# Optimization experiments

Hardware: AMD Instinct MI355X
Metric: run time of the kernel (lower is better)

## Reference

```python
import jax, jax.numpy as jnp
import numpy as np

N = 128           # hidden size n
SIGMA_REC = 0.15  # sigma_rec from __init__


def setup_inputs() -> dict:
    key = jax.random.key(0)
    ks = jax.random.split(key, 6)
    B, T, I, O = 128, 3000, 6, 2
    u = jax.random.normal(ks[0], (B, T, I), jnp.float32)
    p = jax.random.normal(ks[1], (B, N), jnp.float32)
    noise = jax.random.normal(ks[2], (B, T, N), jnp.float32)  # unit normal; scaled in reference
    W_rec = jax.random.normal(ks[3], (N, N), jnp.float32) / jnp.sqrt(jnp.float32(N))
    W_in = jax.random.normal(ks[4], (N, I), jnp.float32) / jnp.sqrt(jnp.float32(I))
    W_out = jax.random.normal(ks[5], (O, N), jnp.float32) / jnp.sqrt(jnp.float32(N))
    alpha = jnp.full((1,), 0.2, jnp.float32)  # dt/tau Euler step
    return dict(u=u, p=p, alpha=alpha, noise=noise, W_rec=W_rec, W_in=W_in, W_out=W_out)


def reference(u, p, alpha, noise, W_rec, W_in, W_out):
    B, T, _ = u.shape
    a = alpha.reshape(())
    scale = jnp.sqrt(2.0 * a * SIGMA_REC ** 2)
    # Precompute the non-recurrent drive for steps 0..T-2, time-major: [T-1, B, N]
    drive = (jnp.einsum('bti,ni->tbn', u[:, :-1], W_in)
             + scale * jnp.swapaxes(noise[:, :-1], 0, 1)
             + p[None, :, :])
    x0 = jnp.zeros((B, N), u.dtype)

    def step(x, d):
        x_new = (1.0 - a) * x + a * jax.nn.relu(x @ W_rec.T + d)
        return x_new, x_new

    _, xs = jax.lax.scan(step, x0, drive)              # xs: [T-1, B, N]
    states = jnp.swapaxes(jnp.concatenate([x0[None], xs], axis=0), 0, 1)  # [B, T, N]
    out = jnp.einsum('btn,on->bto', jax.nn.relu(states), W_out)           # [B, T, 2]
    return out, states
```

## Files before the change

### kernel.cpp

```cpp
#include <hip/hip_runtime.h>
#include <math.h>

#define NH 128
#define NI 6
#define SIGMA_REC 0.15f
#define NCHUNK 8
#define WARM 384

typedef __fp16 h2v __attribute__((ext_vector_type(2)));
typedef unsigned int vu4 __attribute__((ext_vector_type(4)));

__device__ __forceinline__ unsigned int pkh(float a, float b) {
    h2v h = __builtin_amdgcn_cvt_pkrtz(a, b);
    return __builtin_bit_cast(unsigned int, h);
}
#define H2(u) __builtin_bit_cast(h2v, (unsigned int)(u))

struct U6 { float2 a, b, c; };

#define LDWH(r) vu4 w##r##_0, w##r##_1, w##r##_2, w##r##_3, \
                    w##r##_4, w##r##_5, w##r##_6, w##r##_7; { \
    const float4* qp = reinterpret_cast<const float4*>( \
        W_rec + (size_t)(n0 + (r)) * NH + 64 * h); \
    float4 f0 = qp[0],  f1 = qp[1],  f2 = qp[2],  f3 = qp[3]; \
    float4 f4 = qp[4],  f5 = qp[5],  f6 = qp[6],  f7 = qp[7]; \
    float4 f8 = qp[8],  f9 = qp[9],  fA = qp[10], fB = qp[11]; \
    float4 fC = qp[12], fD = qp[13], fE = qp[14], fF = qp[15]; \
    w##r##_0 = (vu4){pkh(f0.x,f0.y), pkh(f0.z,f0.w), pkh(f1.x,f1.y), pkh(f1.z,f1.w)}; \
    w##r##_1 = (vu4){pkh(f2.x,f2.y), pkh(f2.z,f2.w), pkh(f3.x,f3.y), pkh(f3.z,f3.w)}; \
    w##r##_2 = (vu4){pkh(f4.x,f4.y), pkh(f4.z,f4.w), pkh(f5.x,f5.y), pkh(f5.z,f5.w)}; \
    w##r##_3 = (vu4){pkh(f6.x,f6.y), pkh(f6.z,f6.w), pkh(f7.x,f7.y), pkh(f7.z,f7.w)}; \
    w##r##_4 = (vu4){pkh(f8.x,f8.y), pkh(f8.z,f8.w), pkh(f9.x,f9.y), pkh(f9.z,f9.w)}; \
    w##r##_5 = (vu4){pkh(fA.x,fA.y), pkh(fA.z,fA.w), pkh(fB.x,fB.y), pkh(fB.z,fB.w)}; \
    w##r##_6 = (vu4){pkh(fC.x,fC.y), pkh(fC.z,fC.w), pkh(fD.x,fD.y), pkh(fD.z,fD.w)}; \
    w##r##_7 = (vu4){pkh(fE.x,fE.y), pkh(fE.z,fE.w), pkh(fF.x,fF.y), pkh(fF.z,fF.w)}; }

#define ROWDOT(r) h2v acc##r; { \
    h2v t0 = __builtin_elementwise_fma(H2(w##r##_0.x), H2(xh0.x), z2); \
    h2v t1 = __builtin_elementwise_fma(H2(w##r##_0.y), H2(xh0.y), z2); \
    t0 = __builtin_elementwise_fma(H2(w##r##_0.z), H2(xh0.z), t0); \
    t1 = __builtin_elementwise_fma(H2(w##r##_0.w), H2(xh0.w), t1); \
    t0 = __builtin_elementwise_fma(H2(w##r##_1.x), H2(xh1.x), t0); \
    t1 = __builtin_elementwise_fma(H2(w##r##_1.y), H2(xh1.y), t1); \
    t0 = __builtin_elementwise_fma(H2(w##r##_1.z), H2(xh1.z), t0); \
    t1 = __builtin_elementwise_fma(H2(w##r##_1.w), H2(xh1.w), t1); \
    t0 = __builtin_elementwise_fma(H2(w##r##_2.x), H2(xh2.x), t0); \
    t1 = __builtin_elementwise_fma(H2(w##r##_2.y), H2(xh2.y), t1); \
    t0 = __builtin_elementwise_fma(H2(w##r##_2.z), H2(xh2.z), t0); \
    t1 = __builtin_elementwise_fma(H2(w##r##_2.w), H2(xh2.w), t1); \
    t0 = __builtin_elementwise_fma(H2(w##r##_3.x), H2(xh3.x), t0); \
    t1 = __builtin_elementwise_fma(H2(w##r##_3.y), H2(xh3.y), t1); \
    t0 = __builtin_elementwise_fma(H2(w##r##_3.z), H2(xh3.z), t0); \
    t1 = __builtin_elementwise_fma(H2(w##r##_3.w), H2(xh3.w), t1); \
    t0 = __builtin_elementwise_fma(H2(w##r##_4.x), H2(xh4.x), t0); \
    t1 = __builtin_elementwise_fma(H2(w##r##_4.y), H2(xh4.y), t1); \
    t0 = __builtin_elementwise_fma(H2(w##r##_4.z), H2(xh4.z), t0); \
    t1 = __builtin_elementwise_fma(H2(w##r##_4.w), H2(xh4.w), t1); \
    t0 = __builtin_elementwise_fma(H2(w##r##_5.x), H2(xh5.x), t0); \
    t1 = __builtin_elementwise_fma(H2(w##r##_5.y), H2(xh5.y), t1); \
    t0 = __builtin_elementwise_fma(H2(w##r##_5.z), H2(xh5.z), t0); \
    t1 = __builtin_elementwise_fma(H2(w##r##_5.w), H2(xh5.w), t1); \
    t0 = __builtin_elementwise_fma(H2(w##r##_6.x), H2(xh6.x), t0); \
    t1 = __builtin_elementwise_fma(H2(w##r##_6.y), H2(xh6.y), t1); \
    t0 = __builtin_elementwise_fma(H2(w##r##_6.z), H2(xh6.z), t0); \
    t1 = __builtin_elementwise_fma(H2(w##r##_6.w), H2(xh6.w), t1); \
    t0 = __builtin_elementwise_fma(H2(w##r##_7.x), H2(xh7.x), t0); \
    t1 = __builtin_elementwise_fma(H2(w##r##_7.y), H2(xh7.y), t1); \
    t0 = __builtin_elementwise_fma(H2(w##r##_7.z), H2(xh7.z), t0); \
    t1 = __builtin_elementwise_fma(H2(w##r##_7.w), H2(xh7.w), t1); \
    acc##r = t0 + t1; }

#define DOT_OCT(j, xv) \
    c00 = __builtin_amdgcn_fdot2(H2(a##j.x), H2((xv).x), c00, false); \
    c01 = __builtin_amdgcn_fdot2(H2(a##j.y), H2((xv).y), c01, false); \
    c02 = __builtin_amdgcn_fdot2(H2(a##j.z), H2((xv).z), c02, false); \
    c03 = __builtin_amdgcn_fdot2(H2(a##j.w), H2((xv).w), c03, false); \
    c10 = __builtin_amdgcn_fdot2(H2(b##j.x), H2((xv).x), c10, false); \
    c11 = __builtin_amdgcn_fdot2(H2(b##j.y), H2((xv).y), c11, false); \
    c12 = __builtin_amdgcn_fdot2(H2(b##j.z), H2((xv).z), c12, false); \
    c13 = __builtin_amdgcn_fdot2(H2(b##j.w), H2((xv).w), c13, false)

#define LDW(j) vu4 a##j, b##j; { \
    const float4* q0 = reinterpret_cast<const float4*>(wr0 + 8 * (j)); \
    const float4* q1 = reinterpret_cast<const float4*>(wr1 + 8 * (j)); \
    float4 f0 = q0[0], f1 = q0[1], g0 = q1[0], g1 = q1[1]; \
    a##j = (vu4){pkh(f0.x, f0.y), pkh(f0.z, f0.w), pkh(f1.x, f1.y), pkh(f1.z, f1.w)}; \
    b##j = (vu4){pkh(g0.x, g0.y), pkh(g0.z, g0.w), pkh(g1.x, g1.y), pkh(g1.z, g1.w)}; }

#define PIN_AB() \
    asm volatile("" : "+v"(a0), "+v"(a1), "+v"(a2),  "+v"(a3), \
                      "+v"(a4), "+v"(a5), "+v"(a6),  "+v"(a7), \
                      "+v"(a8), "+v"(a9), "+v"(a10), "+v"(a11), \
                      "+v"(a12), "+v"(a13), "+v"(a14), "+v"(a15)); \
    asm volatile("" : "+v"(b0), "+v"(b1), "+v"(b2),  "+v"(b3), \
                      "+v"(b4), "+v"(b5), "+v"(b6),  "+v"(b7), \
                      "+v"(b8), "+v"(b9), "+v"(b10), "+v"(b11), \
                      "+v"(b12), "+v"(b13), "+v"(b14), "+v"(b15))

__global__ __launch_bounds__(256) void drive_kernel(
    const float* __restrict__ u,
    const float* __restrict__ p,
    const float* __restrict__ alpha,
    const float* __restrict__ noise,
    const float* __restrict__ W_in,
    unsigned int* __restrict__ dpre,
    int B, int T)
{
    const float av    = alpha[0];
    const float scale = sqrtf(2.0f * av * SIGMA_REC * SIGMA_REC);
    const size_t total = (size_t)B * T * 64;
    for (size_t idx = (size_t)blockIdx.x * 256 + threadIdx.x; idx < total;
         idx += (size_t)gridDim.x * 256) {
        const int    l  = (int)(idx & 63);
        const size_t bt = idx >> 6;
        const int    b  = (int)(bt / (unsigned)T);
        const int    t  = (int)(bt - (size_t)b * T);

        float2 nz = *reinterpret_cast<const float2*>(
            noise + ((size_t)b * T + t) * NH + 2 * l);
        const float2* ur = reinterpret_cast<const float2*>(
            u + ((size_t)b * T + t) * NI);
        float2 ua = ur[0], ub = ur[1], uc = ur[2];
        const float4* wv = reinterpret_cast<const float4*>(W_in + 2 * l * NI);
        float4 w0 = wv[0], w1 = wv[1], w2 = wv[2];
        float2 pv = *reinterpret_cast<const float2*>(p + (size_t)b * NH + 2 * l);

        float dx = fmaf(ua.x, w0.x, fmaf(ua.y, w0.y, fmaf(ub.x, w0.z,
                   fmaf(ub.y, w0.w, fmaf(uc.x, w1.x, fmaf(uc.y, w1.y,
                   fmaf(scale, nz.x, pv.x)))))));
        float dy = fmaf(ua.x, w1.z, fmaf(ua.y, w1.w, fmaf(ub.x, w2.x,
                   fmaf(ub.y, w2.y, fmaf(uc.x, w2.z, fmaf(uc.y, w2.w,
                   fmaf(scale, nz.y, pv.y)))))));
        dpre[idx] = pkh(dx, dy);
    }
}

__global__ __attribute__((amdgpu_flat_work_group_size(64, 64),
                          amdgpu_waves_per_eu(1, 2)))
void rnn_scan_pre_f(
    const float* __restrict__ W_rec,
    const unsigned int* __restrict__ dpre,
    float* __restrict__ states,
    float* __restrict__ out,
    const float* __restrict__ W_out,
    const float* __restrict__ alpha,
    int T)
{
    const int b     = blockIdx.x;
    const int chunk = blockIdx.y;
    const int lane  = threadIdx.x;
    const int m     = lane & 31;
    const int h     = lane >> 5;
    const int n0    = 4 * m;

    const int NS   = T - 1;
    const int S    = (NS + NCHUNK - 1) / NCHUNK;
    const int s0   = chunk * S;
    const int e0   = min(NS, s0 + S);
    if (s0 >= NS) return;
    const int ws   = max(0, s0 - WARM);
    const int NSm1 = NS - 1;

    __shared__ unsigned int xsh[68];

    LDWH(0) LDWH(1) LDWH(2) LDWH(3)
    asm volatile("" : "+v"(w0_0), "+v"(w0_1), "+v"(w0_2), "+v"(w0_3),
                      "+v"(w0_4), "+v"(w0_5), "+v"(w0_6), "+v"(w0_7),
                      "+v"(w1_0), "+v"(w1_1), "+v"(w1_2), "+v"(w1_3),
                      "+v"(w1_4), "+v"(w1_5), "+v"(w1_6), "+v"(w1_7));
    asm volatile("" : "+v"(w2_0), "+v"(w2_1), "+v"(w2_2), "+v"(w2_3),
                      "+v"(w2_4), "+v"(w2_5), "+v"(w2_6), "+v"(w2_7),
                      "+v"(w3_0), "+v"(w3_1), "+v"(w3_2), "+v"(w3_3),
                      "+v"(w3_4), "+v"(w3_5), "+v"(w3_6), "+v"(w3_7));

    const float av  = alpha[0];
    const float oma = 1.0f - av;

    const float4 wa = *reinterpret_cast<const float4*>(W_out + n0);
    const float4 wb = *reinterpret_cast<const float4*>(W_out + NH + n0);

    const unsigned int* d_b = dpre + (size_t)b * T * 64 + 2 * m;
    float* states_b = states + (size_t)b * T * NH + n0;
    float* out_b    = out + (size_t)b * T * 2;

    const int pidx  = 2 * m + h;
    const int wslot = pidx + ((pidx >= 32) ? 4 : 0);
    xsh[lane + ((lane >= 32) ? 4 : 0)] = 0u;
    if (chunk == 0 && h == 0) {
        *reinterpret_cast<float4*>(states_b) = make_float4(0.f, 0.f, 0.f, 0.f);
        if (m == 0) *reinterpret_cast<float2*>(out_b) = make_float2(0.f, 0.f);
    }
    float xo0 = 0.f, xo1 = 0.f, xo2 = 0.f, xo3 = 0.f;

    auto LDD = [&](int t) {
        return *reinterpret_cast<const uint2*>(d_b + (size_t)t * 64);
    };
    const h2v z2 = {(__fp16)0.f, (__fp16)0.f};

    uint2 dv0 = LDD(min(ws + 0, NSm1)), dv1 = LDD(min(ws + 1, NSm1));
    uint2 dv2 = LDD(min(ws + 2, NSm1)), dv3 = LDD(min(ws + 3, NSm1));
    uint2 dv4 = LDD(min(ws + 4, NSm1)), dv5 = LDD(min(ws + 5, NSm1));
    uint2 dv6 = LDD(min(ws + 6, NSm1)), dv7 = LDD(min(ws + 7, NSm1));

    for (int t = ws; t < e0; ++t) {
        uint2 dn = LDD(min(t + 8, NSm1));
        const vu4* xr = reinterpret_cast<const vu4*>(xsh + h * 36);
        vu4 xh0 = xr[0], xh1 = xr[1], xh2 = xr[2], xh3 = xr[3];
        vu4 xh4 = xr[4], xh5 = xr[5], xh6 = xr[6], xh7 = xr[7];
        ROWDOT(0) ROWDOT(1) ROWDOT(2) ROWDOT(3)
        float f0 = (float)acc0.x + (float)acc0.y;
        float f1 = (float)acc1.x + (float)acc1.y;
        float f2 = (float)acc2.x + (float)acc2.y;
        float f3 = (float)acc3.x + (float)acc3.y;
        int pk01 = (int)pkh(f0, f1), pk23 = (int)pkh(f2, f3);
        h2v q01 = H2((unsigned)__shfl_xor(pk01, 32));
        h2v q23 = H2((unsigned)__shfl_xor(pk23, 32));
        float s0v = f0 + (float)q01.x, s1v = f1 + (float)q01.y;
        float s2v = f2 + (float)q23.x, s3v = f3 + (float)q23.y;
        h2v hd0 = H2(dv0.x), hd1 = H2(dv0.y);
        float xn0 = fmaf(oma, xo0, av * fmaxf(s0v + (float)hd0.x, 0.f));
        float xn1 = fmaf(oma, xo1, av * fmaxf(s1v + (float)hd0.y, 0.f));
        float xn2 = fmaf(oma, xo2, av * fmaxf(s2v + (float)hd1.x, 0.f));
        float xn3 = fmaf(oma, xo3, av * fmaxf(s3v + (float)hd1.y, 0.f));
        xo0 = xn0; xo1 = xn1; xo2 = xn2; xo3 = xn3;
        if (t >= s0) {
            if (h == 0) {
                *reinterpret_cast<float4*>(states_b + (size_t)(t + 1) * NH) =
                    make_float4(xn0, xn1, xn2, xn3);
            }
            float r0 = fmaxf(xn0, 0.f), r1 = fmaxf(xn1, 0.f);
            float r2 = fmaxf(xn2, 0.f), r3 = fmaxf(xn3, 0.f);
            float c0 = fmaf(r0, wa.x, fmaf(r1, wa.y, fmaf(r2, wa.z, r3 * wa.w)));
            float c1 = fmaf(r0, wb.x, fmaf(r1, wb.y, fmaf(r2, wb.z, r3 * wb.w)));
#pragma unroll
            for (int off = 16; off >= 1; off >>= 1) {
                c0 += __shfl_xor(c0, off);
                c1 += __shfl_xor(c1, off);
            }
            if (lane == 0) {
                *reinterpret_cast<float2*>(out_b + (size_t)(t + 1) * 2) =
                    make_float2(c0, c1);
            }
        }
        xsh[wslot] = h ? pkh(xn2, xn3) : pkh(xn0, xn1);
        dv0 = dv1; dv1 = dv2; dv2 = dv3; dv3 = dv4;
        dv4 = dv5; dv5 = dv6; dv6 = dv7; dv7 = dn;
    }
}

__global__ __attribute__((amdgpu_flat_work_group_size(64, 64),
                          amdgpu_waves_per_eu(1, 1)))
void rnn_scan_fb(
    const float* __restrict__ u, const float* __restrict__ p,
    const float* __restrict__ alpha, const float* __restrict__ noise,
    const float* __restrict__ W_rec, const float* __restrict__ W_in,
    float* __restrict__ states, int T)
{
    const int b    = blockIdx.x;
    const int lane = threadIdx.x;
    const int n0   = lane * 2;

    __shared__ unsigned int xsh[64];

    const float* wr0 = W_rec + (size_t)n0 * NH;
    const float* wr1 = wr0 + NH;
    LDW(0)  LDW(1)  LDW(2)  LDW(3)  LDW(4)  LDW(5)  LDW(6)  LDW(7)
    LDW(8)  LDW(9)  LDW(10) LDW(11) LDW(12) LDW(13) LDW(14) LDW(15)
    PIN_AB();

    const float wiA0 = W_in[n0 * NI + 0], wiA1 = W_in[n0 * NI + 1];
    const float wiA2 = W_in[n0 * NI + 2], wiA3 = W_in[n0 * NI + 3];
    const float wiA4 = W_in[n0 * NI + 4], wiA5 = W_in[n0 * NI + 5];
    const float wiB0 = W_in[(n0 + 1) * NI + 0], wiB1 = W_in[(n0 + 1) * NI + 1];
    const float wiB2 = W_in[(n0 + 1) * NI + 2], wiB3 = W_in[(n0 + 1) * NI + 3];
    const float wiB4 = W_in[(n0 + 1) * NI + 4], wiB5 = W_in[(n0 + 1) * NI + 5];

    const float2 pn   = *reinterpret_cast<const float2*>(p + (size_t)b * NH + n0);
    const float av    = alpha[0];
    const float oma   = 1.0f - av;
    const float scale = sqrtf(2.0f * av * SIGMA_REC * SIGMA_REC);

    const float* noise_b = noise + (size_t)b * T * NH + n0;
    unsigned int zv;
    asm volatile("v_mov_b32 %0, 0" : "=v"(zv));
    const float* u_b = u + (size_t)b * T * NI + zv;
    float* st_ptr = states + (size_t)b * T * NH + n0 + NH;

    xsh[lane] = 0u;
    *reinterpret_cast<float2*>(states + (size_t)b * T * NH + n0) = make_float2(0.f, 0.f);
    float xo0 = 0.0f, xo1 = 0.0f;

    auto LDnz = [&](int t) {
        return *reinterpret_cast<const float2*>(noise_b + (size_t)t * NH);
    };
    auto loadU = [&](int t) {
        const float2* up = reinterpret_cast<const float2*>(u_b + (size_t)t * NI);
        U6 r; r.a = up[0]; r.b = up[1]; r.c = up[2]; return r;
    };
    auto mkd = [&](float2 nz, const U6& uu) {
        float dx = fmaf(uu.a.x, wiA0, fmaf(uu.a.y, wiA1, fmaf(uu.b.x, wiA2,
                   fmaf(uu.b.y, wiA3, fmaf(uu.c.x, wiA4, fmaf(uu.c.y, wiA5,
                   fmaf(scale, nz.x, pn.x)))))));
        float dy = fmaf(uu.a.x, wiB0, fmaf(uu.a.y, wiB1, fmaf(uu.b.x, wiB2,
                   fmaf(uu.b.y, wiB3, fmaf(uu.c.x, wiB4, fmaf(uu.c.y, wiB5,
                   fmaf(scale, nz.y, pn.y)))))));
        return make_float2(dx, dy);
    };
    auto step = [&](float2 d) {
        const vu4* xr = reinterpret_cast<const vu4*>(xsh);
        float c00 = 0.f, c01 = 0.f, c02 = 0.f, c03 = 0.f;
        float c10 = 0.f, c11 = 0.f, c12 = 0.f, c13 = 0.f;
        vu4 xv0 = xr[0], xv1 = xr[1], xv2 = xr[2], xv3 = xr[3];
        vu4 xv4 = xr[4], xv5 = xr[5], xv6 = xr[6], xv7 = xr[7];
        DOT_OCT(0, xv0);  DOT_OCT(1, xv1);  DOT_OCT(2, xv2);  DOT_OCT(3, xv3);
        vu4 xv8 = xr[8], xv9 = xr[9], xv10 = xr[10], xv11 = xr[11];
        DOT_OCT(4, xv4);  DOT_OCT(5, xv5);  DOT_OCT(6, xv6);  DOT_OCT(7, xv7);
        vu4 xv12 = xr[12], xv13 = xr[13], xv14 = xr[14], xv15 = xr[15];
        DOT_OCT(8, xv8);  DOT_OCT(9, xv9);  DOT_OCT(10, xv10); DOT_OCT(11, xv11);
        DOT_OCT(12, xv12); DOT_OCT(13, xv13); DOT_OCT(14, xv14); DOT_OCT(15, xv15);
        float pre0 = ((c00 + c01) + (c02 + c03)) + d.x;
        float pre1 = ((c10 + c11) + (c12 + c13)) + d.y;
        float xn0 = fmaf(oma, xo0, av * fmaxf(pre0, 0.f));
        float xn1 = fmaf(oma, xo1, av * fmaxf(pre1, 0.f));
        xo0 = xn0; xo1 = xn1;
        *reinterpret_cast<float2*>(st_ptr) = make_float2(xn0, xn1);
        st_ptr += NH;
        xsh[lane] = pkh(xn0, xn1);
    };

    float2 nz0 = LDnz(0), nz1 = LDnz(1), nz2 = LDnz(2), nz3 = LDnz(3);
    U6 u0 = loadU(0), u1 = loadU(1), u2 = loadU(2), u3 = loadU(3);
    float2 nzA0 = LDnz(4), nzA1 = LDnz(5);   U6 uA0 = loadU(4), uA1 = loadU(5);
    float2 nzB0 = LDnz(6), nzB1 = LDnz(7);   U6 uB0 = loadU(6), uB1 = loadU(7);
    float2 d0 = mkd(nz0, u0), d1 = mkd(nz1, u1);
    float2 d2 = mkd(nz2, u2), d3 = mkd(nz3, u3);

    int t = 0;
    for (; t + 1 < T - 1; t += 2) {
        const int t8 = min(t + 8, T - 1), t9 = min(t + 9, T - 1);
        float2 nzC0 = LDnz(t8), nzC1 = LDnz(t9);
        U6 uC0 = loadU(t8), uC1 = loadU(t9);
        float2 dE = mkd(nzA0, uA0), dF = mkd(nzA1, uA1);
        step(d0);
        step(d1);
        d0 = d2; d1 = d3; d2 = dE; d3 = dF;
        nzA0 = nzB0; nzA1 = nzB1; uA0 = uB0; uA1 = uB1;
        nzB0 = nzC0; nzB1 = nzC1; uB0 = uC0; uB1 = uC1;
    }
    if (t < T - 1) step(d0);
}

__global__ __launch_bounds__(256) void out_proj_kernel(
    const float* __restrict__ states,
    const float* __restrict__ W_out,
    float* __restrict__ out,
    int rows)
{
    const int wave = threadIdx.x >> 6;
    const int lane = threadIdx.x & 63;
    const int l    = lane & 31;
    const int row  = blockIdx.x * 8 + wave * 2 + (lane >> 5);
    if (row >= rows) return;

    float4 s = *reinterpret_cast<const float4*>(states + (size_t)row * NH + l * 4);
    s.x = fmaxf(s.x, 0.f); s.y = fmaxf(s.y, 0.f);
    s.z = fmaxf(s.z, 0.f); s.w = fmaxf(s.w, 0.f);
    float4 wa = reinterpret_cast<const float4*>(W_out)[l];
    float4 wb = reinterpret_cast<const float4*>(W_out + NH)[l];
    float c0 = s.x * wa.x + s.y * wa.y + s.z * wa.z + s.w * wa.w;
    float c1 = s.x * wb.x + s.y * wb.y + s.z * wb.z + s.w * wb.w;

#pragma unroll
    for (int off = 16; off >= 1; off >>= 1) {
        c0 += __shfl_xor(c0, off);
        c1 += __shfl_xor(c1, off);
    }
    if (l == 0) {
        *reinterpret_cast<float2*>(out + (size_t)row * 2) = make_float2(c0, c1);
    }
}

extern "C" void kernel_launch(void* const* d_in, const int* in_sizes, int n_in,
                              void* d_out, int out_size, void* d_ws, size_t ws_size,
                              hipStream_t stream) {
    const float* u     = (const float*)d_in[0];
    const float* p     = (const float*)d_in[1];
    const float* alpha = (const float*)d_in[2];
    const float* noise = (const float*)d_in[3];
    const float* W_rec = (const float*)d_in[4];
    const float* W_in  = (const float*)d_in[5];
    const float* W_out = (const float*)d_in[6];

    const int B = in_sizes[1] / NH;
    const int T = in_sizes[0] / (B * NI);

    float* out    = (float*)d_out;
    float* states = out + (size_t)B * T * 2;

    const size_t need = (size_t)B * T * 64 * sizeof(unsigned int);
    if (d_ws != nullptr && ws_size >= need) {
        unsigned int* dpre = (unsigned int*)d_ws;
        drive_kernel<<<2048, 256, 0, stream>>>(u, p, alpha, noise, W_in,
                                               dpre, B, T);
        dim3 grid(B, NCHUNK);
        rnn_scan_pre_f<<<grid, 64, 0, stream>>>(W_rec, dpre, states, out,
                                                W_out, alpha, T);
    } else {
        rnn_scan_fb<<<B, 64, 0, stream>>>(u, p, alpha, noise, W_rec, W_in,
                                          states, T);
        const int rows = B * T;
        out_proj_kernel<<<(rows + 7) / 8, 256, 0, stream>>>(states, W_out,
                                                            out, rows);
    }
}
```

Measured before the change: 626.8 us.

## Defer output projection by one step and interleave its reductions with row dots

The W_out projection for the previous step's state is now computed at the start of the next iteration, and its shuffle reductions are interleaved between the ROWDOT blocks. The aim is to take the readout off the recurrent critical path and hide shuffle latency behind the matvec FMAs. Each half-wave (h) now computes only one of the two outputs, so one reduction replaces two and the W_out register use is halved. A tail block after the loop writes the final step's output. This adds an extra relu/FMA per step during warmup iterations and relies on the t > s0 boundary handling being correct.

Measured after the change: 668.3 us. +6.6%, slower.

```diff
diff --git a/kernel.cpp b/kernel.cpp
--- a/kernel.cpp
+++ b/kernel.cpp
@@ -176,8 +176,7 @@
     const float av  = alpha[0];
     const float oma = 1.0f - av;
 
-    const float4 wa = *reinterpret_cast<const float4*>(W_out + n0);
-    const float4 wb = *reinterpret_cast<const float4*>(W_out + NH + n0);
+    const float4 wsel = *reinterpret_cast<const float4*>(W_out + h * NH + n0);
 
     const unsigned int* d_b = dpre + (size_t)b * T * 64 + 2 * m;
     float* states_b = states + (size_t)b * T * NH + n0;
@@ -207,7 +206,22 @@
         const vu4* xr = reinterpret_cast<const vu4*>(xsh + h * 36);
         vu4 xh0 = xr[0], xh1 = xr[1], xh2 = xr[2], xh3 = xr[3];
         vu4 xh4 = xr[4], xh5 = xr[5], xh6 = xr[6], xh7 = xr[7];
-        ROWDOT(0) ROWDOT(1) ROWDOT(2) ROWDOT(3)
+        float pr0 = fmaxf(xo0, 0.f), pr1 = fmaxf(xo1, 0.f);
+        float pr2 = fmaxf(xo2, 0.f), pr3 = fmaxf(xo3, 0.f);
+        float pc = fmaf(pr0, wsel.x, fmaf(pr1, wsel.y,
+                   fmaf(pr2, wsel.z, pr3 * wsel.w)));
+        ROWDOT(0)
+        pc += __shfl_xor(pc, 16);
+        ROWDOT(1)
+        pc += __shfl_xor(pc, 8);
+        ROWDOT(2)
+        pc += __shfl_xor(pc, 4);
+        ROWDOT(3)
+        pc += __shfl_xor(pc, 2);
+        pc += __shfl_xor(pc, 1);
+        if (m == 0 && t > s0) {
+            out_b[(size_t)t * 2 + h] = pc;
+        }
         float f0 = (float)acc0.x + (float)acc0.y;
         float f1 = (float)acc1.x + (float)acc1.y;
         float f2 = (float)acc2.x + (float)acc2.y;
@@ -223,28 +237,25 @@
         float xn2 = fmaf(oma, xo2, av * fmaxf(s2v + (float)hd1.x, 0.f));
         float xn3 = fmaf(oma, xo3, av * fmaxf(s3v + (float)hd1.y, 0.f));
         xo0 = xn0; xo1 = xn1; xo2 = xn2; xo3 = xn3;
-        if (t >= s0) {
-            if (h == 0) {
-                *reinterpret_cast<float4*>(states_b + (size_t)(t + 1) * NH) =
-                    make_float4(xn0, xn1, xn2, xn3);
-            }
-            float r0 = fmaxf(xn0, 0.f), r1 = fmaxf(xn1, 0.f);
-            float r2 = fmaxf(xn2, 0.f), r3 = fmaxf(xn3, 0.f);
-            float c0 = fmaf(r0, wa.x, fmaf(r1, wa.y, fmaf(r2, wa.z, r3 * wa.w)));
-            float c1 = fmaf(r0, wb.x, fmaf(r1, wb.y, fmaf(r2, wb.z, r3 * wb.w)));
-#pragma unroll
-            for (int off = 16; off >= 1; off >>= 1) {
-                c0 += __shfl_xor(c0, off);
-                c1 += __shfl_xor(c1, off);
-            }
-            if (lane == 0) {
-                *reinterpret_cast<float2*>(out_b + (size_t)(t + 1) * 2) =
-                    make_float2(c0, c1);
-            }
+        if (t >= s0 && h == 0) {
+            *reinterpret_cast<float4*>(states_b + (size_t)(t + 1) * NH) =
+                make_float4(xn0, xn1, xn2, xn3);
         }
         xsh[wslot] = h ? pkh(xn2, xn3) : pkh(xn0, xn1);
         dv0 = dv1; dv1 = dv2; dv2 = dv3; dv3 = dv4;
         dv4 = dv5; dv5 = dv6; dv6 = dv7; dv7 = dn;
+    }
+
+    {
+        float pr0 = fmaxf(xo0, 0.f), pr1 = fmaxf(xo1, 0.f);
+        float pr2 = fmaxf(xo2, 0.f), pr3 = fmaxf(xo3, 0.f);
+        float pc = fmaf(pr0, wsel.x, fmaf(pr1, wsel.y,
+                   fmaf(pr2, wsel.z, pr3 * wsel.w)));
+#pragma unroll
+        for (int off = 16; off >= 1; off >>= 1) pc += __shfl_xor(pc, off);
+        if (m == 0) {
+            out_b[(size_t)e0 * 2 + h] = pc;
+        }
     }
 }
 
```
